# Kernel tuning notes

Measured on AMD Instinct MI355X. Metric: run time of the kernel, lower is better.

The kernel has to match this reference:

```python
import jax, jax.numpy as jnp
import numpy as np

D_MODEL = 1024
N_HEADS = 16
D_K = D_MODEL // N_HEADS
THETA = 10000.0
MAX_SEQ = 2048


def _trunc_normal(key, shape, std):
    # approximate trunc_normal in [-3std, 3std] via clipping (init only; values irrelevant to math)
    return jnp.clip(jax.random.normal(key, shape) * std, -3 * std, 3 * std).astype(jnp.float32)


def setup_inputs() -> dict:
    key = jax.random.key(0)
    kx, kq, kk, kv, ko = jax.random.split(key, 5)
    std = np.sqrt(2.0 / (D_MODEL + D_MODEL))
    x = jax.random.normal(kx, (2, 2048, D_MODEL), dtype=jnp.float32)
    W_q = _trunc_normal(kq, (D_MODEL, D_MODEL), std)
    W_k = _trunc_normal(kk, (D_MODEL, D_MODEL), std)
    W_v = _trunc_normal(kv, (D_MODEL, D_MODEL), std)
    W_o = _trunc_normal(ko, (D_MODEL, D_MODEL), std)
    return {"x": x, "W_q": W_q, "W_k": W_k, "W_v": W_v, "W_o": W_o}


def _rope(x, positions):
    # x: [b, n, s, d_k]; interleaved even/odd pairing: (x0,x1),(x2,x3),...
    d = x.shape[-1]
    inv_freq = THETA ** (-2.0 * jnp.arange(0, d // 2, dtype=jnp.float32) / d)
    angles = positions.astype(jnp.float32)[:, None] * inv_freq[None, :]  # [s, d/2]
    cos, sin = jnp.cos(angles), jnp.sin(angles)
    xp = x.reshape(x.shape[:-1] + (d // 2, 2))
    x_even, x_odd = xp[..., 0], xp[..., 1]
    out_even = x_even * cos - x_odd * sin
    out_odd = x_even * sin + x_odd * cos
    return jnp.stack((out_even, out_odd), axis=-1).reshape(x.shape)


def reference(x, W_q, W_k, W_v, W_o):
    b, s, _ = x.shape
    def split_heads(t):
        return t.reshape(b, s, N_HEADS, D_K).transpose(0, 2, 1, 3)  # b n s d
    Q = split_heads(x @ W_q.T)
    K = split_heads(x @ W_k.T)
    V = split_heads(x @ W_v.T)
    pos = jnp.arange(s)
    Q = _rope(Q, pos)
    K = _rope(K, pos)
    score = jnp.einsum('bnqd,bnkd->bnqk', Q, K) / jnp.sqrt(jnp.float32(D_K))
    causal = jnp.triu(jnp.ones((s, s), dtype=bool), k=1)
    score = jnp.where(causal[None, None], -jnp.inf, score)
    attn = jax.nn.softmax(score, axis=-1)
    out = jnp.einsum('bnqk,bnkd->bnqd', attn, V)
    out = out.transpose(0, 2, 1, 3).reshape(b, s, D_MODEL)
    return out @ W_o.T
```

## Files before the change

kernel.cpp:

```cpp
#include <hip/hip_runtime.h>

typedef float f32x4 __attribute__((ext_vector_type(4)));
typedef __bf16 bf16x8 __attribute__((ext_vector_type(8)));

#define D_MODEL 1024
#define SEQ     2048
#define NB      2
#define NH      16
#define DK      64

__device__ __forceinline__ unsigned short f2bf(float f) {
    union { float f; unsigned int u; } un; un.f = f;
    unsigned int r = un.u + 0x7fffu + ((un.u >> 16) & 1u);
    return (unsigned short)(r >> 16);
}

__device__ __forceinline__ unsigned cvtpk(float lo, float hi) {
    unsigned r;
    asm("v_cvt_pk_bf16_f32 %0, %1, %2" : "=v"(r) : "v"(lo), "v"(hi));
    return r;
}

__device__ __forceinline__ void gload16(const void* g, void* l) {
    __builtin_amdgcn_global_load_lds((__attribute__((address_space(1))) void*)g,
                                     (__attribute__((address_space(3))) void*)l,
                                     16, 0, 0);
}

__global__ __launch_bounds__(256) void cast5(
    const float* __restrict__ x,  const float* __restrict__ wq,
    const float* __restrict__ wk, const float* __restrict__ wv,
    const float* __restrict__ wo,
    unsigned short* __restrict__ xb,  unsigned short* __restrict__ wqb,
    unsigned short* __restrict__ wkb, unsigned short* __restrict__ wvb,
    unsigned short* __restrict__ wob, float2* __restrict__ tab)
{
    if (blockIdx.y == 5) {
        int idx = blockIdx.x * 256 + threadIdx.x;
        if (idx < SEQ * 32) {
            int ss = idx >> 5, p = idx & 31;
            float freq = exp2f(-0.41524101186f * (float)p);
            float sn, cs;
            sincosf((float)ss * freq, &sn, &cs);
            tab[idx] = make_float2(cs, sn);
        }
        return;
    }
    const float* src; unsigned short* dst; int n8;
    switch (blockIdx.y) {
        case 0:  src = x;  dst = xb;  n8 = (NB*SEQ*D_MODEL)/8; break;
        case 1:  src = wq; dst = wqb; n8 = (D_MODEL*D_MODEL)/8; break;
        case 2:  src = wk; dst = wkb; n8 = (D_MODEL*D_MODEL)/8; break;
        case 3:  src = wv; dst = wvb; n8 = (D_MODEL*D_MODEL)/8; break;
        default: src = wo; dst = wob; n8 = (D_MODEL*D_MODEL)/8; break;
    }
    int stride = gridDim.x * blockDim.x;
    for (int i = blockIdx.x * blockDim.x + threadIdx.x; i < n8; i += stride) {
        const float4* p = (const float4*)src + (size_t)i * 2;
        float4 a = p[0], b = p[1];
        union { unsigned short h[8]; uint4 v; } u;
        u.h[0] = f2bf(a.x); u.h[1] = f2bf(a.y); u.h[2] = f2bf(a.z); u.h[3] = f2bf(a.w);
        u.h[4] = f2bf(b.x); u.h[5] = f2bf(b.y); u.h[6] = f2bf(b.z); u.h[7] = f2bf(b.w);
        ((uint4*)dst)[i] = u.v;
    }
}

template <int MODE>
__global__ __launch_bounds__(256) void gemm_bt(
    const unsigned short* __restrict__ A,
    const unsigned short* __restrict__ B0,
    const unsigned short* __restrict__ B1,
    const unsigned short* __restrict__ B2,
    float* __restrict__ outF,
    unsigned short* __restrict__ Qh,
    unsigned short* __restrict__ Kh,
    unsigned short* __restrict__ Vt,
    const float2* __restrict__ tab,
    int M, int K)
{
    __shared__ unsigned short As[128 * 32];
    __shared__ unsigned short Bs[128 * 32];

    const int lane = threadIdx.x & 63;
    const int wid  = threadIdx.x >> 6;
    const int l15 = lane & 15, lhi = lane >> 4;
    const int m0 = blockIdx.y * 128;
    const int n0 = blockIdx.x * 128;
    const int z  = (MODE == 1) ? (int)blockIdx.z : 0;
    const unsigned short* B = (z == 0) ? B0 : (z == 1) ? B1 : B2;
    const int waveM = (wid >> 1) * 64;
    const int waveN = (wid & 1) * 64;

    f32x4 acc[4][4];
    f32x4 zero = {0.f, 0.f, 0.f, 0.f};
#pragma unroll
    for (int m = 0; m < 4; ++m)
#pragma unroll
        for (int n = 0; n < 4; ++n) acc[m][n] = zero;

    const int lrow = lane >> 2;
    const int lcol = (lane & 3) * 8;

    for (int k0 = 0; k0 < K; k0 += 32) {
#pragma unroll
        for (int q = 0; q < 2; ++q) {
            int rbase = wid * 32 + q * 16;
            const unsigned short* gA = A + (size_t)(m0 + rbase + lrow) * K + k0 + lcol;
            gload16(gA, (char*)As + rbase * 64);
            const unsigned short* gB = B + (size_t)(n0 + rbase + lrow) * K + k0 + lcol;
            gload16(gB, (char*)Bs + rbase * 64);
        }
        __syncthreads();
        bf16x8 af[4], bfr[4];
#pragma unroll
        for (int m = 0; m < 4; ++m)
            af[m] = *(const bf16x8*)(As + (waveM + m * 16 + l15) * 32 + lhi * 8);
#pragma unroll
        for (int n = 0; n < 4; ++n)
            bfr[n] = *(const bf16x8*)(Bs + (waveN + n * 16 + l15) * 32 + lhi * 8);
#pragma unroll
        for (int m = 0; m < 4; ++m)
#pragma unroll
            for (int n = 0; n < 4; ++n)
                acc[m][n] = __builtin_amdgcn_mfma_f32_16x16x32_bf16(af[m], bfr[n], acc[m][n], 0, 0, 0);
        __syncthreads();
    }

    if constexpr (MODE == 0) {
#pragma unroll
        for (int n = 0; n < 4; ++n) {
            int col = n0 + waveN + n * 16 + l15;
#pragma unroll
            for (int m = 0; m < 4; ++m) {
                int rowb = m0 + waveM + m * 16 + (lhi << 2);
#pragma unroll
                for (int r = 0; r < 4; ++r)
                    outF[(size_t)(rowb + r) * D_MODEL + col] = acc[m][n][r];
            }
        }
    } else {
        __shared__ unsigned short Ct[4][64][72];
        const int colg0 = n0 + waveN;
        const int hh    = (colg0 >> 6) & (NH - 1);
        const int rowg0 = m0 + waveM;
        const int bb    = rowg0 >> 11;
        const size_t bhh = (size_t)(bb * NH + hh);

#pragma unroll
        for (int n = 0; n < 4; ++n) {
            int cl = n * 16 + l15;
#pragma unroll
            for (int m = 0; m < 4; ++m) {
#pragma unroll
                for (int r = 0; r < 4; ++r) {
                    float v  = acc[m][n][r];
                    float pv = __shfl_xor(v, 1);
                    int rl = m * 16 + (lhi << 2) + r;
                    if (z == 2) {
                        Ct[wid][cl][rl] = f2bf(v);
                    } else {
                        int ss = (rowg0 + rl) & (SEQ - 1);
                        float2 cs = tab[(ss << 5) + (cl >> 1)];
                        float o = (cl & 1) ? (pv * cs.y + v * cs.x)
                                           : (v * cs.x - pv * cs.y);
                        if (z == 0) o *= 0.18033688011f;
                        Ct[wid][rl][cl] = f2bf(o);
                    }
                }
            }
        }
        asm volatile("s_waitcnt lgkmcnt(0)" ::: "memory");

        const int lr = lane >> 3;
        const int lc = (lane & 7) << 3;
#pragma unroll
        for (int i = 0; i < 8; ++i) {
            int rl = i * 8 + lr;
            uint4 w = *(const uint4*)&Ct[wid][rl][lc];
            if (z == 2) {
                int ss0 = rowg0 & (SEQ - 1);
                *(uint4*)(Vt + (bhh * DK + rl) * SEQ + ss0 + lc) = w;
            } else {
                int ss = (rowg0 + rl) & (SEQ - 1);
                unsigned short* dst = (z == 0) ? Qh : Kh;
                *(uint4*)(dst + (bhh * SEQ + ss) * DK + lc) = w;
            }
        }
    }
}

__global__ __launch_bounds__(256) void attn_kernel(
    const unsigned short* __restrict__ Qh,
    const unsigned short* __restrict__ Kh,
    const unsigned short* __restrict__ Vt,
    unsigned short* __restrict__ O)
{
    __shared__ unsigned short Ks[2][64 * 64];
    __shared__ unsigned short Vs[2][64 * 64];
    __shared__ unsigned short P[4][16 * 64];

    const int tid  = threadIdx.x;
    const int lane = tid & 63;
    const int wid  = tid >> 6;
    const int l15 = lane & 15, lhi = lane >> 4;
    const int bh = blockIdx.x;
    const int pi = blockIdx.y;
    const int b = bh >> 4, h = bh & 15;

    const unsigned short* Qb = Qh + (size_t)bh * SEQ * DK;
    const unsigned short* Kb = Kh + (size_t)bh * SEQ * DK;
    const unsigned short* Vb = Vt + (size_t)bh * DK * SEQ;

    auto STAGE = [&](int buf, int kv0s) {
#pragma unroll
        for (int c = 0; c < 2; ++c) {
            int ub = c * 256 + wid * 64;
            int u  = ub + lane;
            int kr = u >> 3;
            int kc = (u & 7) ^ (kr & 7);
            gload16(Kb + (size_t)(kv0s + kr) * DK + kc * 8, &Ks[buf][(size_t)(ub + lane) * 8 - (size_t)lane * 8 + (size_t)lane * 8]);
        }
#pragma unroll
        for (int c = 0; c < 2; ++c) {
            int ub = c * 256 + wid * 64;
            int u  = ub + lane;
            int vr = u >> 3;
            int vc = (u & 7) ^ (vr & 7);
            gload16(Vb + (size_t)vr * SEQ + kv0s + vc * 8, &Vs[buf][(size_t)u * 8]);
        }
    };

    const f32x4 zero = {0.f, 0.f, 0.f, 0.f};
    const f32x4 ninf = {-1e30f, -1e30f, -1e30f, -1e30f};

    STAGE(0, 0);
    int cur = 0;

    for (int ph = 0; ph < 2; ++ph) {
        const int qt = ph ? (31 - pi) : pi;
        const int ktl = qt;
        const int q0 = qt * 64;
        const int qw = q0 + wid * 16;

        bf16x8 qf[2];
#pragma unroll
        for (int kk = 0; kk < 2; ++kk)
            qf[kk] = *(const bf16x8*)(Qb + (size_t)(qw + l15) * DK + kk * 32 + lhi * 8);

        f32x4 oacc[4];
#pragma unroll
        for (int nd = 0; nd < 4; ++nd) oacc[nd] = zero;
        float mrow = -1e30f;
        float lrow = 0.f;

        for (int kt = 0; kt <= ktl; ++kt) {
            const int kv0 = kt << 6;
            const bool diag = (kt == ktl);
            const int nlim = diag ? (wid + 1) : 4;

            asm volatile("s_waitcnt vmcnt(0)" ::: "memory");
            __builtin_amdgcn_s_barrier();
            __builtin_amdgcn_sched_barrier(0);

            const bool hasNext = (kt < ktl) || (ph == 0);
            if (hasNext) STAGE(cur ^ 1, (kt < ktl) ? (kv0 + 64) : 0);

            f32x4 s[4];
#pragma unroll
            for (int n = 0; n < 4; ++n) s[n] = (n < nlim) ? zero : ninf;

            const int sw = l15 & 7;
            __builtin_amdgcn_s_setprio(1);
#pragma unroll
            for (int n = 0; n < 4; ++n) {
                if (n < nlim) {
                    int r = n * 16 + l15;
                    bf16x8 k0 = *(const bf16x8*)&Ks[cur][r * 64 + ((lhi ^ sw) << 3)];
                    bf16x8 k1 = *(const bf16x8*)&Ks[cur][r * 64 + (((4 + lhi) ^ sw) << 3)];
                    s[n] = __builtin_amdgcn_mfma_f32_16x16x32_bf16(k0, qf[0], s[n], 0, 0, 0);
                    s[n] = __builtin_amdgcn_mfma_f32_16x16x32_bf16(k1, qf[1], s[n], 0, 0, 0);
                }
            }
            __builtin_amdgcn_s_setprio(0);

            if (diag) {
                const int qg = qw + l15;
#pragma unroll
                for (int n = 0; n < 4; ++n) {
                    if (n < nlim) {
#pragma unroll
                        for (int r = 0; r < 4; ++r) {
                            int kg = kv0 + n * 16 + (lhi << 2) + r;
                            if (kg > qg) s[n][r] = -1e30f;
                        }
                    }
                }
            }

            float mx = fmaxf(fmaxf(s[0][0], s[0][1]), fmaxf(s[0][2], s[0][3]));
#pragma unroll
            for (int n = 1; n < 4; ++n)
                mx = fmaxf(mx, fmaxf(fmaxf(s[n][0], s[n][1]), fmaxf(s[n][2], s[n][3])));
            mx = fmaxf(mx, __shfl_xor(mx, 16));
            mx = fmaxf(mx, __shfl_xor(mx, 32));

            float alpha = 1.f;
            const int allDefer = __all(mx <= mrow + 8.f);
            if (!allDefer) {
                float mn = fmaxf(mrow, mx);
                alpha = __builtin_amdgcn_exp2f(mrow - mn);
                mrow = mn;
            }

#pragma unroll
            for (int n = 0; n < 4; ++n)
#pragma unroll
                for (int r = 0; r < 4; ++r)
                    s[n][r] = __builtin_amdgcn_exp2f(s[n][r] - mrow);

            float rs = 0.f;
#pragma unroll
            for (int n = 0; n < 4; ++n)
                rs += (s[n][0] + s[n][1]) + (s[n][2] + s[n][3]);
            rs += __shfl_xor(rs, 16);
            rs += __shfl_xor(rs, 32);
            lrow = allDefer ? (lrow + rs) : (lrow * alpha + rs);

#pragma unroll
            for (int n = 0; n < 4; ++n) {
                uint2 pk;
                pk.x = cvtpk(s[n][0], s[n][1]);
                pk.y = cvtpk(s[n][2], s[n][3]);
                int cW = 2 * n + (lhi >> 1);
                *(uint2*)&P[wid][(l15 << 6) + ((cW ^ sw) << 3) + ((lhi & 1) << 2)] = pk;
            }

            if (!allDefer) {
                float a0 = __shfl(alpha, (lhi << 2) + 0);
                float a1 = __shfl(alpha, (lhi << 2) + 1);
                float a2 = __shfl(alpha, (lhi << 2) + 2);
                float a3 = __shfl(alpha, (lhi << 2) + 3);
#pragma unroll
                for (int nd = 0; nd < 4; ++nd) {
                    oacc[nd][0] *= a0; oacc[nd][1] *= a1;
                    oacc[nd][2] *= a2; oacc[nd][3] *= a3;
                }
            }

            asm volatile("s_waitcnt lgkmcnt(0)" ::: "memory");
            const int kklim = diag ? ((nlim + 1) >> 1) : 2;
            bf16x8 pa[2];
#pragma unroll
            for (int kk = 0; kk < 2; ++kk)
                if (kk < kklim)
                    pa[kk] = *(const bf16x8*)&P[wid][(l15 << 6) + ((((kk << 2) + lhi) ^ sw) << 3)];

            __builtin_amdgcn_s_setprio(1);
#pragma unroll
            for (int nd = 0; nd < 4; ++nd)
#pragma unroll
                for (int kk = 0; kk < 2; ++kk)
                    if (kk < kklim) {
                        int rd = nd * 16 + l15;
                        bf16x8 vf = *(const bf16x8*)&Vs[cur][rd * 64 + ((((kk << 2) + lhi) ^ sw) << 3)];
                        oacc[nd] = __builtin_amdgcn_mfma_f32_16x16x32_bf16(pa[kk], vf, oacc[nd], 0, 0, 0);
                    }
            __builtin_amdgcn_s_setprio(0);

            cur ^= 1;
        }

        float inv = 1.f / lrow;
        float i0 = __shfl(inv, (lhi << 2) + 0);
        float i1 = __shfl(inv, (lhi << 2) + 1);
        float i2 = __shfl(inv, (lhi << 2) + 2);
        float i3 = __shfl(inv, (lhi << 2) + 3);
#pragma unroll
        for (int nd = 0; nd < 4; ++nd) {
            int d = nd * 16 + l15;
            int rowb = qw + (lhi << 2);
            O[((size_t)(b * SEQ + rowb + 0)) * D_MODEL + h * DK + d] = f2bf(oacc[nd][0] * i0);
            O[((size_t)(b * SEQ + rowb + 1)) * D_MODEL + h * DK + d] = f2bf(oacc[nd][1] * i1);
            O[((size_t)(b * SEQ + rowb + 2)) * D_MODEL + h * DK + d] = f2bf(oacc[nd][2] * i2);
            O[((size_t)(b * SEQ + rowb + 3)) * D_MODEL + h * DK + d] = f2bf(oacc[nd][3] * i3);
        }
    }
}

extern "C" void kernel_launch(void* const* d_in, const int* in_sizes, int n_in,
                              void* d_out, int out_size, void* d_ws, size_t ws_size,
                              hipStream_t stream)
{
    const float* x  = (const float*)d_in[0];
    const float* Wq = (const float*)d_in[1];
    const float* Wk = (const float*)d_in[2];
    const float* Wv = (const float*)d_in[3];
    const float* Wo = (const float*)d_in[4];
    float* out = (float*)d_out;

    char* ws = (char*)d_ws;
    unsigned short* xb  = (unsigned short*)(ws);
    unsigned short* Wqb = (unsigned short*)(ws + ( 8ull << 20));
    unsigned short* Wkb = (unsigned short*)(ws + (10ull << 20));
    unsigned short* Wvb = (unsigned short*)(ws + (12ull << 20));
    unsigned short* Wob = (unsigned short*)(ws + (14ull << 20));
    unsigned short* Qh  = (unsigned short*)(ws + (16ull << 20));
    unsigned short* Kh  = (unsigned short*)(ws + (24ull << 20));
    unsigned short* Vt  = (unsigned short*)(ws + (32ull << 20));
    float2*         tab = (float2*)(ws + (40ull << 20));
    unsigned short* attn = xb;

    cast5<<<dim3(512, 6), 256, 0, stream>>>(x, Wq, Wk, Wv, Wo, xb, Wqb, Wkb, Wvb, Wob, tab);

    gemm_bt<1><<<dim3(D_MODEL / 128, (NB * SEQ) / 128, 3), 256, 0, stream>>>(
        xb, Wqb, Wkb, Wvb, nullptr, Qh, Kh, Vt, tab, NB * SEQ, D_MODEL);

    attn_kernel<<<dim3(NB * NH, 16), 256, 0, stream>>>(Qh, Kh, Vt, attn);

    gemm_bt<0><<<dim3(D_MODEL / 128, (NB * SEQ) / 128, 1), 256, 0, stream>>>(
        attn, Wob, Wob, Wob, out, nullptr, nullptr, nullptr, nullptr, NB * SEQ, D_MODEL);
}
```

Measured before the change: 130.5 us.

## Triple-buffer GEMM LDS tiles with async prefetch and one barrier per step

The bf16 GEMM kernel now keeps three LDS stages and issues async global-to-LDS loads two k-steps ahead. It uses vmcnt waits and a single s_barrier per iteration in place of two __syncthreads, so memory latency can overlap with the MFMA work. MFMA sections are raised in priority with s_setprio, and the epilogue transpose buffer is aliased onto the stage buffers to keep LDS use bounded. The attention kernel's global_load_lds destinations are simplified to wave-uniform bases. The costs are higher LDS use per block, which may lower occupancy, and reliance on hand-counted vmcnt correctness.

```diff
diff --git a/kernel.cpp b/kernel.cpp
--- a/kernel.cpp
+++ b/kernel.cpp
@@ -78,8 +78,7 @@
     const float2* __restrict__ tab,
     int M, int K)
 {
-    __shared__ unsigned short As[128 * 32];
-    __shared__ unsigned short Bs[128 * 32];
+    __shared__ __align__(16) unsigned short SM[3][2][128 * 32];
 
     const int lane = threadIdx.x & 63;
     const int wid  = threadIdx.x >> 6;
@@ -101,29 +100,44 @@
     const int lrow = lane >> 2;
     const int lcol = (lane & 3) * 8;
 
-    for (int k0 = 0; k0 < K; k0 += 32) {
+    auto STAGE = [&](int buf, int k0) {
 #pragma unroll
         for (int q = 0; q < 2; ++q) {
             int rbase = wid * 32 + q * 16;
-            const unsigned short* gA = A + (size_t)(m0 + rbase + lrow) * K + k0 + lcol;
-            gload16(gA, (char*)As + rbase * 64);
-            const unsigned short* gB = B + (size_t)(n0 + rbase + lrow) * K + k0 + lcol;
-            gload16(gB, (char*)Bs + rbase * 64);
-        }
-        __syncthreads();
+            gload16(A + (size_t)(m0 + rbase + lrow) * K + k0 + lcol,
+                    (char*)&SM[buf][0][0] + rbase * 64);
+            gload16(B + (size_t)(n0 + rbase + lrow) * K + k0 + lcol,
+                    (char*)&SM[buf][1][0] + rbase * 64);
+        }
+    };
+
+    const int NK = K >> 5;
+    STAGE(0, 0);
+    STAGE(1, 32);
+
+    for (int k = 0; k < NK; ++k) {
+        if (k < NK - 1) asm volatile("s_waitcnt vmcnt(4)" ::: "memory");
+        else            asm volatile("s_waitcnt vmcnt(0)" ::: "memory");
+        __builtin_amdgcn_s_barrier();
+        __builtin_amdgcn_sched_barrier(0);
+        if (k + 2 < NK) STAGE((k + 2) % 3, (k + 2) << 5);
+
+        const unsigned short* as = SM[k % 3][0];
+        const unsigned short* bs = SM[k % 3][1];
         bf16x8 af[4], bfr[4];
 #pragma unroll
         for (int m = 0; m < 4; ++m)
-            af[m] = *(const bf16x8*)(As + (waveM + m * 16 + l15) * 32 + lhi * 8);
+            af[m] = *(const bf16x8*)(as + (waveM + m * 16 + l15) * 32 + lhi * 8);
 #pragma unroll
         for (int n = 0; n < 4; ++n)
-            bfr[n] = *(const bf16x8*)(Bs + (waveN + n * 16 + l15) * 32 + lhi * 8);
+            bfr[n] = *(const bf16x8*)(bs + (waveN + n * 16 + l15) * 32 + lhi * 8);
+        __builtin_amdgcn_s_setprio(1);
 #pragma unroll
         for (int m = 0; m < 4; ++m)
 #pragma unroll
             for (int n = 0; n < 4; ++n)
                 acc[m][n] = __builtin_amdgcn_mfma_f32_16x16x32_bf16(af[m], bfr[n], acc[m][n], 0, 0, 0);
-        __syncthreads();
+        __builtin_amdgcn_s_setprio(0);
     }
 
     if constexpr (MODE == 0) {
@@ -139,7 +153,8 @@
             }
         }
     } else {
-        __shared__ unsigned short Ct[4][64][72];
+        __syncthreads();
+        unsigned short* Ct = ((unsigned short*)SM) + wid * 4608;
         const int colg0 = n0 + waveN;
         const int hh    = (colg0 >> 6) & (NH - 1);
         const int rowg0 = m0 + waveM;
@@ -157,14 +172,14 @@
                     float pv = __shfl_xor(v, 1);
                     int rl = m * 16 + (lhi << 2) + r;
                     if (z == 2) {
-                        Ct[wid][cl][rl] = f2bf(v);
+                        Ct[cl * 72 + rl] = f2bf(v);
                     } else {
                         int ss = (rowg0 + rl) & (SEQ - 1);
                         float2 cs = tab[(ss << 5) + (cl >> 1)];
                         float o = (cl & 1) ? (pv * cs.y + v * cs.x)
                                            : (v * cs.x - pv * cs.y);
                         if (z == 0) o *= 0.18033688011f;
-                        Ct[wid][rl][cl] = f2bf(o);
+                        Ct[rl * 72 + cl] = f2bf(o);
                     }
                 }
             }
@@ -176,7 +191,7 @@
 #pragma unroll
         for (int i = 0; i < 8; ++i) {
             int rl = i * 8 + lr;
-            uint4 w = *(const uint4*)&Ct[wid][rl][lc];
+            uint4 w = *(const uint4*)&Ct[rl * 72 + lc];
             if (z == 2) {
                 int ss0 = rowg0 & (SEQ - 1);
                 *(uint4*)(Vt + (bhh * DK + rl) * SEQ + ss0 + lc) = w;
@@ -218,7 +233,7 @@
             int u  = ub + lane;
             int kr = u >> 3;
             int kc = (u & 7) ^ (kr & 7);
-            gload16(Kb + (size_t)(kv0s + kr) * DK + kc * 8, &Ks[buf][(size_t)(ub + lane) * 8 - (size_t)lane * 8 + (size_t)lane * 8]);
+            gload16(Kb + (size_t)(kv0s + kr) * DK + kc * 8, &Ks[buf][(size_t)ub * 8]);
         }
 #pragma unroll
         for (int c = 0; c < 2; ++c) {
@@ -226,7 +241,7 @@
             int u  = ub + lane;
             int vr = u >> 3;
             int vc = (u & 7) ^ (vr & 7);
-            gload16(Vb + (size_t)vr * SEQ + kv0s + vc * 8, &Vs[buf][(size_t)u * 8]);
+            gload16(Vb + (size_t)vr * SEQ + kv0s + vc * 8, &Vs[buf][(size_t)ub * 8]);
         }
     };
 
```

After: 118.9 us. 1.1x faster.
